# Kernel optimization log

Measured on AMD Instinct MI355X. Metric: run time of the kernel, lower is better.

The kernel has to match this reference:

```python
import jax, jax.numpy as jnp
import numpy as np

N_NODES = 2000
GCN_OUT = 8
HID = 256
N_STEPS_OUT = 4


def setup_inputs() -> dict:
    key = jax.random.key(0)
    ks = jax.random.split(key, 16)
    B, S, N, E, F, H = 32, 24, N_NODES, 16000, GCN_OUT, HID
    I = F * N  # LSTM input size = gcn_out_features * num_nodes
    s = 0.05
    inp = {
        "x_sequences": jax.random.normal(ks[0], (B, S, N), jnp.float32),
        "edge_index": jax.random.randint(ks[1], (B, S, 2, E), 0, N, jnp.int32),
        "edge_distances": jax.random.uniform(ks[2], (B, S, E), jnp.float32),
        # CustomGCNLayer params (linear 1->F)
        "W_gcn": jax.random.normal(ks[3], (1, F), jnp.float32) * s,
        "b_gcn": jnp.zeros((F,), jnp.float32),
        # 2-layer LSTM (PyTorch layout: [4H, in], gate order i,f,g,o)
        "Wih0": jax.random.normal(ks[4], (4 * H, I), jnp.float32) * s,
        "Whh0": jax.random.normal(ks[5], (4 * H, H), jnp.float32) * s,
        "bih0": jnp.zeros((4 * H,), jnp.float32),
        "bhh0": jnp.zeros((4 * H,), jnp.float32),
        "Wih1": jax.random.normal(ks[6], (4 * H, H), jnp.float32) * s,
        "Whh1": jax.random.normal(ks[7], (4 * H, H), jnp.float32) * s,
        "bih1": jnp.zeros((4 * H,), jnp.float32),
        "bhh1": jnp.zeros((4 * H,), jnp.float32),
        # fc: hidden -> n_steps_out * num_nodes * num_node_features
        "fc_W": jax.random.normal(ks[8], (N_STEPS_OUT * N, H), jnp.float32) * s,
        "fc_b": jnp.zeros((N_STEPS_OUT * N,), jnp.float32),
    }
    return inp


def _lstm_layer(x, Wih, Whh, bih, bhh):
    # x: [B, S, in] -> hs: [B, S, H]
    B = x.shape[0]
    H = Whh.shape[1]
    b = bih + bhh

    def step(carry, xt):
        h, c = carry
        gates = xt @ Wih.T + h @ Whh.T + b  # [B, 4H]
        i, f, g, o = jnp.split(gates, 4, axis=-1)
        i = jax.nn.sigmoid(i)
        f = jax.nn.sigmoid(f)
        g = jnp.tanh(g)
        o = jax.nn.sigmoid(o)
        c = f * c + i * g
        h = o * jnp.tanh(c)
        return (h, c), h

    init = (jnp.zeros((B, H), x.dtype), jnp.zeros((B, H), x.dtype))
    _, hs = jax.lax.scan(step, init, x.transpose(1, 0, 2))  # time-major
    return hs.transpose(1, 0, 2)


def reference(x_sequences, edge_index, edge_distances, W_gcn, b_gcn,
              Wih0, Whh0, bih0, bhh0, Wih1, Whh1, bih1, bhh1, fc_W, fc_b):
    B, S, N = x_sequences.shape
    F = W_gcn.shape[1]
    # GCN layer (batched over all B*S graph snapshots):
    # h = x @ W + b ; out[i] = sum_{(j->i)} dist_e * h[j]
    h = x_sequences[..., None] * W_gcn[0] + b_gcn        # [B,S,N,F]
    src = edge_index[:, :, 0].reshape(B * S, -1)         # [BS,E]
    dst = edge_index[:, :, 1].reshape(B * S, -1)
    dist = edge_distances.reshape(B * S, -1)
    h2 = h.reshape(B * S, N, F)
    msgs = jnp.take_along_axis(h2, src[:, :, None], axis=1) * dist[..., None]  # [BS,E,F]
    agg = jax.vmap(lambda m, d: jax.ops.segment_sum(m, d, num_segments=N))(msgs, dst)
    gcn_seq = jnp.tanh(agg.reshape(B, S, N * F))         # [B,S,N*F]

    h1 = _lstm_layer(gcn_seq, Wih0, Whh0, bih0, bhh0)
    h2l = _lstm_layer(h1, Wih1, Whh1, bih1, bhh1)
    last = jnp.tanh(h2l)[:, -1, :]                       # [B,H]
    out = last @ fc_W.T + fc_b                           # [B, n_steps_out*N]
    n_steps_out = fc_b.shape[0] // N
    return out.reshape(B, n_steps_out, N)                # num_node_features=1 squeezed
```

## Files before the change

kernel.cpp:

```cpp
#include <hip/hip_runtime.h>

#define DEVINL __device__ __forceinline__

typedef __attribute__((ext_vector_type(8))) short bf16x8;
typedef __attribute__((ext_vector_type(4))) float f32x4;
typedef _Float16 half2_t __attribute__((ext_vector_type(2)));
typedef _Float16 f16x8 __attribute__((ext_vector_type(8)));

DEVINL unsigned short f2bf(float f) {
  unsigned int u = __float_as_uint(f);
  u += 0x7FFFu + ((u >> 16) & 1u);
  return (unsigned short)(u >> 16);
}
DEVINL unsigned short f2h(float f) {
  return __builtin_bit_cast(unsigned short, (_Float16)f);
}
DEVINL float sigmf(float x) { return 1.f / (1.f + __expf(-x)); }
DEVINL float tanh_fast(float x) { float e = __expf(2.f * x); return 1.f - 2.f / (e + 1.f); }

DEVINL float fdot2u(unsigned int h, unsigned int w, float acc) {
  return __builtin_amdgcn_fdot2(__builtin_bit_cast(half2_t, h),
                                __builtin_bit_cast(half2_t, w), acc, false);
}

DEVINL void gload_lds16(const void* g, void* l) {
  __builtin_amdgcn_global_load_lds(
      (const __attribute__((address_space(1))) void*)g,
      (__attribute__((address_space(3))) void*)l, 16, 0, 0);
}

#define FXSCALE 1048576.f
#define FXINV   (1.f / 1048576.f)

__global__ __launch_bounds__(1024) void fused_pre(
    const float* __restrict__ x, const int* __restrict__ ei, const float* __restrict__ ed,
    const float* __restrict__ Wg, const float* __restrict__ bg,
    unsigned short* __restrict__ G,
    const float* __restrict__ Wih0, unsigned short* __restrict__ W0bf,
    const float* __restrict__ Whh0, uint2* __restrict__ WPG0,
    const float* __restrict__ Whh1, uint2* __restrict__ WPG1,
    const float* __restrict__ Wih1, unsigned short* __restrict__ W1h) {
  __shared__ float xs[2000];
  __shared__ int Ai[2000];
  __shared__ int Di[2000];
  int blk = blockIdx.x;
  int tid = threadIdx.x;

  if (blk < 768) {
    int bs = blk;
    for (int i = tid; i < 2000; i += 1024) {
      xs[i] = x[(size_t)bs * 2000 + i];
      Ai[i] = 0; Di[i] = 0;
    }
    bool bgz = (bg[0] == 0.f) && (bg[1] == 0.f) && (bg[2] == 0.f) && (bg[3] == 0.f) &&
               (bg[4] == 0.f) && (bg[5] == 0.f) && (bg[6] == 0.f) && (bg[7] == 0.f);
    __syncthreads();
    const int4* srcp = (const int4*)(ei + (size_t)bs * 32000);
    const int4* dstp = (const int4*)(ei + (size_t)bs * 32000 + 16000);
    const float4* dp = (const float4*)(ed + (size_t)bs * 16000);
    if (bgz) {
      for (int i = tid; i < 4000; i += 1024) {
        int4 s4 = srcp[i];
        int4 d4 = dstp[i];
        float4 w4 = dp[i];
        atomicAdd(&Ai[d4.x], __float2int_rn(w4.x * xs[s4.x] * FXSCALE));
        atomicAdd(&Ai[d4.y], __float2int_rn(w4.y * xs[s4.y] * FXSCALE));
        atomicAdd(&Ai[d4.z], __float2int_rn(w4.z * xs[s4.z] * FXSCALE));
        atomicAdd(&Ai[d4.w], __float2int_rn(w4.w * xs[s4.w] * FXSCALE));
      }
    } else {
      for (int i = tid; i < 4000; i += 1024) {
        int4 s4 = srcp[i];
        int4 d4 = dstp[i];
        float4 w4 = dp[i];
        atomicAdd(&Ai[d4.x], __float2int_rn(w4.x * xs[s4.x] * FXSCALE));
        atomicAdd(&Di[d4.x], __float2int_rn(w4.x * FXSCALE));
        atomicAdd(&Ai[d4.y], __float2int_rn(w4.y * xs[s4.y] * FXSCALE));
        atomicAdd(&Di[d4.y], __float2int_rn(w4.y * FXSCALE));
        atomicAdd(&Ai[d4.z], __float2int_rn(w4.z * xs[s4.z] * FXSCALE));
        atomicAdd(&Di[d4.z], __float2int_rn(w4.z * FXSCALE));
        atomicAdd(&Ai[d4.w], __float2int_rn(w4.w * xs[s4.w] * FXSCALE));
        atomicAdd(&Di[d4.w], __float2int_rn(w4.w * FXSCALE));
      }
    }
    __syncthreads();
    float wreg[8], breg[8];
#pragma unroll
    for (int f = 0; f < 8; ++f) { wreg[f] = Wg[f]; breg[f] = bg[f]; }
    for (int n = tid; n < 2000; n += 1024) {
      float a  = (float)Ai[n] * FXINV;
      float dd = (float)Di[n] * FXINV;
      unsigned int u[4];
#pragma unroll
      for (int p = 0; p < 4; ++p) {
        float v0 = tanh_fast(wreg[2 * p] * a + breg[2 * p] * dd);
        float v1 = tanh_fast(wreg[2 * p + 1] * a + breg[2 * p + 1] * dd);
        u[p] = (unsigned int)f2bf(v0) | ((unsigned int)f2bf(v1) << 16);
      }
      *(uint4*)&G[(size_t)bs * 16000 + n * 8] = make_uint4(u[0], u[1], u[2], u[3]);
    }
  } else if (blk < 1768) {
    int base = (blk - 768) * 1024 + tid;
#pragma unroll
    for (int k = 0; k < 4; ++k) {
      int id = base + k * 1024000;
      float4 v = *(const float4*)&Wih0[(size_t)id * 4];
      unsigned int a = (unsigned int)f2bf(v.x) | ((unsigned int)f2bf(v.y) << 16);
      unsigned int b = (unsigned int)f2bf(v.z) | ((unsigned int)f2bf(v.w) << 16);
      *(uint2*)&W0bf[(size_t)id * 4] = make_uint2(a, b);
    }
  } else if (blk < 1896) {
    const float* in = (blk < 1832) ? Whh0 : Whh1;
    uint2* outp = (blk < 1832) ? WPG0 : WPG1;
    int id = ((blk < 1832) ? (blk - 1768) : (blk - 1832)) * 1024 + tid;
    int g = id >> 14;
    int rem = id & 16383;
    int u2 = rem >> 8;
    int c = rem & 255;
    int col = (c >> 6) * 256 + g * 64 + (c & 63);
    float4 v = *(const float4*)&in[col * 256 + u2 * 4];
    unsigned int p0 = (unsigned int)f2h(v.x) | ((unsigned int)f2h(v.y) << 16);
    unsigned int p1 = (unsigned int)f2h(v.z) | ((unsigned int)f2h(v.w) << 16);
    outp[id] = make_uint2(p0, p1);
  } else {
    int id = (blk - 1896) * 1024 + tid;
    W1h[id] = f2h(Wih1[id]);
  }
}

__global__ __launch_bounds__(256) void gemm_bt(
    const unsigned short* __restrict__ A, const unsigned short* __restrict__ B,
    float* __restrict__ Cp) {
  __shared__ __align__(16) unsigned short As[2][128 * 32];
  __shared__ __align__(16) unsigned short Bs[2][128 * 32];
  const int K = 16000;
  int nt = blockIdx.x;
  int mt = blockIdx.y;
  int ks = blockIdx.z;
  int m0 = mt * 128, n0 = nt * 128;
  int tid = threadIdx.x;
  int lane = tid & 63;
  int w = tid >> 6;
  int wm = (w >> 1) * 64, wn = (w & 1) * 64;
  int fr = lane & 15;
  int kg = lane >> 4;

  f32x4 acc[4][4] = {};
  const unsigned short* Ag = A + (size_t)m0 * K + ks * 1600;
  const unsigned short* Bg = B + (size_t)n0 * K + ks * 1600;

  int row0 = tid >> 2,            ko0 = (tid & 3) * 8,        cb0 = (tid & ~63);
  int row1 = (256 + tid) >> 2,    ko1 = (tid & 3) * 8,        cb1 = 256 + (tid & ~63);

#define STAGE_BT(buf, kk)                                                     \
  do {                                                                        \
    gload_lds16(&Ag[(size_t)row0 * K + (kk) + ko0], &As[buf][cb0 * 8]);       \
    gload_lds16(&Bg[(size_t)row0 * K + (kk) + ko0], &Bs[buf][cb0 * 8]);       \
    gload_lds16(&Ag[(size_t)row1 * K + (kk) + ko1], &As[buf][cb1 * 8]);       \
    gload_lds16(&Bg[(size_t)row1 * K + (kk) + ko1], &Bs[buf][cb1 * 8]);       \
  } while (0)

  STAGE_BT(0, 0);
#pragma unroll 1
  for (int it = 0; it < 50; ++it) {
    int cur = it & 1;
    if (it < 49) {
      STAGE_BT(cur ^ 1, (it + 1) * 32);
      asm volatile("s_waitcnt vmcnt(4)" ::: "memory");
    } else {
      asm volatile("s_waitcnt vmcnt(0)" ::: "memory");
    }
    __builtin_amdgcn_s_barrier();
    __builtin_amdgcn_sched_barrier(0);
    bf16x8 aF[4], bF[4];
#pragma unroll
    for (int i = 0; i < 4; ++i)
      aF[i] = *(const bf16x8*)&As[cur][(wm + i * 16 + fr) * 32 + kg * 8];
#pragma unroll
    for (int i = 0; i < 4; ++i)
      bF[i] = *(const bf16x8*)&Bs[cur][(wn + i * 16 + fr) * 32 + kg * 8];
#pragma unroll
    for (int i = 0; i < 4; ++i)
#pragma unroll
      for (int j = 0; j < 4; ++j)
        acc[i][j] = __builtin_amdgcn_mfma_f32_16x16x32_bf16(aF[i], bF[j], acc[i][j], 0, 0, 0);
    __builtin_amdgcn_s_barrier();
  }
#undef STAGE_BT
  float* Co = Cp + (size_t)ks * 768 * 1024;
  int mr = (lane >> 4) * 4;
#pragma unroll
  for (int i = 0; i < 4; ++i)
#pragma unroll
    for (int j = 0; j < 4; ++j) {
      int n = n0 + wn + j * 16 + fr;
#pragma unroll
      for (int r = 0; r < 4; ++r) {
        int m = m0 + wm + i * 16 + mr + r;
        Co[(size_t)m * 1024 + n] = acc[i][j][r];
      }
    }
}

__global__ __launch_bounds__(1024) void lstm_sync2(
    const float* __restrict__ Z, const float* __restrict__ Cp,
    const float* __restrict__ bih, const float* __restrict__ bhh,
    const uint2* __restrict__ WPG,
    unsigned int* __restrict__ Hex, unsigned short* __restrict__ Hout,
    float* __restrict__ lastOut, int tagBase) {
  __shared__ __align__(16) uint2 Wl2[64 * 256];
  __shared__ float gparts[1024];
  __shared__ __align__(8) unsigned short h16[256];
  int bid = blockIdx.x;
  int b = bid & 31, g = bid >> 5;
  int tid = threadIdx.x;
  int lane = tid & 63;
  int c = tid & 255;
  int kh = __builtin_amdgcn_readfirstlane(tid >> 8);
  int q = c >> 6, r = c & 63;
  int col = q * 256 + g * 64 + r;

  const uint2* wsrc = WPG + (size_t)g * 16384;
  for (int i = tid; i < 16384; i += 1024) Wl2[i] = wsrc[i];
  if (tid < 128) ((unsigned int*)h16)[tid] = 0;
  float biasc = (Cp != nullptr && kh == 0) ? (bih[col] + bhh[col]) : 0.f;
  __syncthreads();

  float cst = 0.f;
  const size_t b24 = (size_t)b * 24;

#pragma unroll 1
  for (int t = 0; t < 24; ++t) {
    uint2 hv = *(const uint2*)&((const unsigned int*)h16)[lane * 2];
    float z = 0.f;
    if (kh == 0) {
      if (Cp != nullptr) {
        size_t off = (b24 + t) * 1024 + col;
        float s = biasc;
#pragma unroll
        for (int p = 0; p < 10; ++p) s += Cp[(size_t)p * 786432 + off];
        z = s;
      } else {
        z = Z[(b24 + t) * 1024 + col];
      }
    }
    float acc = 0.f;
#pragma unroll
    for (int j = 0; j < 16; ++j) {
      const int u2i = kh * 16 + j;
      uint2 w2 = Wl2[u2i * 256 + c];
      unsigned int h0 = (unsigned int)__builtin_amdgcn_readlane((int)hv.x, u2i);
      unsigned int h1 = (unsigned int)__builtin_amdgcn_readlane((int)hv.y, u2i);
      acc = fdot2u(h0, w2.x, acc);
      acc = fdot2u(h1, w2.y, acc);
    }
    gparts[tid] = acc + z;
    __syncthreads();
    unsigned int* HexS = Hex + (t & 1) * 8192 + b * 256;
    if (tid < 64) {
      float i_ = gparts[tid]       + gparts[tid + 256]  + gparts[tid + 512]  + gparts[tid + 768];
      float f_ = gparts[tid + 64]  + gparts[tid + 320]  + gparts[tid + 576]  + gparts[tid + 832];
      float g_ = gparts[tid + 128] + gparts[tid + 384]  + gparts[tid + 640]  + gparts[tid + 896];
      float o_ = gparts[tid + 192] + gparts[tid + 448]  + gparts[tid + 704]  + gparts[tid + 960];
      float ig = sigmf(i_), fg = sigmf(f_);
      float gg = tanh_fast(g_), og = sigmf(o_);
      cst = fg * cst + ig * gg;
      float h = og * tanh_fast(cst);
      unsigned short hh = f2h(h);
      h16[g * 64 + tid] = hh;
      __hip_atomic_store(&HexS[g * 64 + tid],
                         (unsigned int)hh | ((unsigned int)(tagBase + t + 1) << 16),
                         __ATOMIC_RELAXED, __HIP_MEMORY_SCOPE_AGENT);
      if (Hout) Hout[(b24 + t) * 256 + g * 64 + tid] = hh;
      if (lastOut && t == 23) lastOut[b * 256 + g * 64 + tid] = tanh_fast(h);
    }
    if (t == 23) break;
    if (tid < 256 && (tid >> 6) != g) {
      const unsigned int tag = (unsigned int)(tagBase + t + 1);
      unsigned int v;
      do {
        v = __hip_atomic_load(&HexS[tid], __ATOMIC_RELAXED, __HIP_MEMORY_SCOPE_AGENT);
      } while ((v >> 16) != tag);
      h16[tid] = (unsigned short)(v & 0xFFFFu);
    }
    __syncthreads();
  }
}

__global__ __launch_bounds__(256) void gemm_z1_mfma(
    const unsigned short* __restrict__ A, const unsigned short* __restrict__ B,
    const float* __restrict__ bih, const float* __restrict__ bhh,
    float* __restrict__ Z1) {
  __shared__ __align__(16) unsigned short As[128 * 32];
  __shared__ __align__(16) unsigned short Bs[128 * 32];
  const int K = 256;
  int nt = blockIdx.x;
  int mt = blockIdx.y;
  int m0 = mt * 128, n0 = nt * 128;
  int tid = threadIdx.x;
  int lane = tid & 63;
  int w = tid >> 6;
  int wm = (w >> 1) * 64, wn = (w & 1) * 64;
  int fr = lane & 15;
  int kg = lane >> 4;

  f32x4 acc[4][4] = {};
  const unsigned short* Ag = A + (size_t)m0 * K;
  const unsigned short* Bg = B + (size_t)n0 * K;

  for (int kk = 0; kk < 256; kk += 32) {
#pragma unroll
    for (int q = 0; q < 2; ++q) {
      int c = q * 256 + tid;
      int row = c >> 2;
      int ko = (c & 3) * 8;
      int cb = q * 256 + (tid & ~63);
      gload_lds16(&Ag[(size_t)row * K + kk + ko], &As[cb * 8]);
      gload_lds16(&Bg[(size_t)row * K + kk + ko], &Bs[cb * 8]);
    }
    __syncthreads();
    f16x8 aF[4], bF[4];
#pragma unroll
    for (int i = 0; i < 4; ++i)
      aF[i] = *(const f16x8*)&As[(wm + i * 16 + fr) * 32 + kg * 8];
#pragma unroll
    for (int i = 0; i < 4; ++i)
      bF[i] = *(const f16x8*)&Bs[(wn + i * 16 + fr) * 32 + kg * 8];
#pragma unroll
    for (int i = 0; i < 4; ++i)
#pragma unroll
      for (int j = 0; j < 4; ++j)
        acc[i][j] = __builtin_amdgcn_mfma_f32_16x16x32_f16(aF[i], bF[j], acc[i][j], 0, 0, 0);
    __syncthreads();
  }
  int mr = (lane >> 4) * 4;
#pragma unroll
  for (int j = 0; j < 4; ++j) {
    int n = n0 + wn + j * 16 + fr;
    float bias = bih[n] + bhh[n];
#pragma unroll
    for (int i = 0; i < 4; ++i) {
#pragma unroll
      for (int r = 0; r < 4; ++r) {
        int m = m0 + wm + i * 16 + mr + r;
        Z1[(size_t)m * 1024 + n] = acc[i][j][r] + bias;
      }
    }
  }
}

__global__ __launch_bounds__(256) void fc_kernel(
    const float* __restrict__ last, const float* __restrict__ fcW,
    const float* __restrict__ fcb, float* __restrict__ out) {
  __shared__ float ls[8][256];
  int tid = threadIdx.x;
  int o = blockIdx.x * 256 + tid;
  int b0 = blockIdx.y * 8;
  for (int i = tid; i < 2048; i += 256)
    ls[i >> 8][i & 255] = last[(b0 + (i >> 8)) * 256 + (i & 255)];
  __syncthreads();
  if (o < 8000) {
    float acc[8] = {};
    for (int k = 0; k < 256; k += 4) {
      float4 wv = *(const float4*)&fcW[(size_t)o * 256 + k];
#pragma unroll
      for (int b = 0; b < 8; ++b)
        acc[b] += wv.x * ls[b][k] + wv.y * ls[b][k + 1] + wv.z * ls[b][k + 2] + wv.w * ls[b][k + 3];
    }
    float bias = fcb[o];
#pragma unroll
    for (int b = 0; b < 8; ++b) out[(size_t)(b0 + b) * 8000 + o] = acc[b] + bias;
  }
}

extern "C" void kernel_launch(void* const* d_in, const int* in_sizes, int n_in,
                              void* d_out, int out_size, void* d_ws, size_t ws_size,
                              hipStream_t stream) {
  const float* x    = (const float*)d_in[0];
  const int*   ei   = (const int*)d_in[1];
  const float* ed   = (const float*)d_in[2];
  const float* Wg   = (const float*)d_in[3];
  const float* bg   = (const float*)d_in[4];
  const float* Wih0 = (const float*)d_in[5];
  const float* Whh0 = (const float*)d_in[6];
  const float* bih0 = (const float*)d_in[7];
  const float* bhh0 = (const float*)d_in[8];
  const float* Wih1 = (const float*)d_in[9];
  const float* Whh1 = (const float*)d_in[10];
  const float* bih1 = (const float*)d_in[11];
  const float* bhh1 = (const float*)d_in[12];
  const float* fcW  = (const float*)d_in[13];
  const float* fcb  = (const float*)d_in[14];
  float* out = (float*)d_out;

  char* ws = (char*)d_ws;
  unsigned short* Gbf  = (unsigned short*)(ws);
  unsigned short* W0bf = (unsigned short*)(ws + 24576000);
  float* Zpart = (float*)(ws + 57344000);
  uint2* WPG0  = (uint2*)(ws + 91947008);
  uint2* WPG1  = (uint2*)(ws + 92471296);
  unsigned short* W1h = (unsigned short*)(ws + 92995584);
  unsigned short* H1  = (unsigned short*)(ws + 94044160);
  float* Z1    = (float*)(ws + 94830592);
  float* lastb = (float*)(ws + 97976320);
  unsigned int* Hex0 = (unsigned int*)(ws + 98009088);
  unsigned int* Hex1 = (unsigned int*)(ws + 98074624);

  hipMemsetAsync(Hex0, 0, 131072, stream);
  fused_pre<<<2152, 1024, 0, stream>>>(x, ei, ed, Wg, bg, Gbf,
                                       Wih0, W0bf, Whh0, WPG0, Whh1, WPG1,
                                       Wih1, (unsigned short*)W1h);
  gemm_bt<<<dim3(8, 6, 10), 256, 0, stream>>>(Gbf, W0bf, Zpart);
  lstm_sync2<<<128, 1024, 0, stream>>>(nullptr, Zpart, bih0, bhh0, WPG0,
                                       Hex0, H1, nullptr, 0);
  gemm_z1_mfma<<<dim3(8, 6), 256, 0, stream>>>(H1, W1h, bih1, bhh1, Z1);
  lstm_sync2<<<128, 1024, 0, stream>>>(Z1, nullptr, nullptr, nullptr, WPG1,
                                       Hex1, nullptr, lastb, 100);
  fc_kernel<<<dim3(32, 4), 256, 0, stream>>>(lastb, fcW, fcb, out);
}
```

Baseline: 231.2 us.

## Fuse Wih0 fp32-to-bf16 conversion into the input-projection GEMM B loads

Removes the separate pass in the preprocessing kernel that converted the 1024x16000 fp32 Wih0 into a bf16 workspace copy. The GEMM now loads fp32 B tiles into registers, converts them to bf16, and writes them to LDS itself, using an extra wait and barrier per iteration. This saves the write and reread of a 32 MB bf16 buffer. In exchange, each GEMM block reads twice as many bytes for B, Wih0 is reread by all 6 M-tile blocks in fp32, and the register-staged path with an extra barrier may pipeline less well than the direct-to-LDS loads.

Result: slower. 247.2 us (+6.9%).

```diff
diff --git a/kernel.cpp b/kernel.cpp
--- a/kernel.cpp
+++ b/kernel.cpp
@@ -36,7 +36,6 @@
     const float* __restrict__ x, const int* __restrict__ ei, const float* __restrict__ ed,
     const float* __restrict__ Wg, const float* __restrict__ bg,
     unsigned short* __restrict__ G,
-    const float* __restrict__ Wih0, unsigned short* __restrict__ W0bf,
     const float* __restrict__ Whh0, uint2* __restrict__ WPG0,
     const float* __restrict__ Whh1, uint2* __restrict__ WPG1,
     const float* __restrict__ Wih1, unsigned short* __restrict__ W1h) {
@@ -99,20 +98,10 @@
       }
       *(uint4*)&G[(size_t)bs * 16000 + n * 8] = make_uint4(u[0], u[1], u[2], u[3]);
     }
-  } else if (blk < 1768) {
-    int base = (blk - 768) * 1024 + tid;
-#pragma unroll
-    for (int k = 0; k < 4; ++k) {
-      int id = base + k * 1024000;
-      float4 v = *(const float4*)&Wih0[(size_t)id * 4];
-      unsigned int a = (unsigned int)f2bf(v.x) | ((unsigned int)f2bf(v.y) << 16);
-      unsigned int b = (unsigned int)f2bf(v.z) | ((unsigned int)f2bf(v.w) << 16);
-      *(uint2*)&W0bf[(size_t)id * 4] = make_uint2(a, b);
-    }
-  } else if (blk < 1896) {
-    const float* in = (blk < 1832) ? Whh0 : Whh1;
-    uint2* outp = (blk < 1832) ? WPG0 : WPG1;
-    int id = ((blk < 1832) ? (blk - 1768) : (blk - 1832)) * 1024 + tid;
+  } else if (blk < 896) {
+    const float* in = (blk < 832) ? Whh0 : Whh1;
+    uint2* outp = (blk < 832) ? WPG0 : WPG1;
+    int id = ((blk < 832) ? (blk - 768) : (blk - 832)) * 1024 + tid;
     int g = id >> 14;
     int rem = id & 16383;
     int u2 = rem >> 8;
@@ -123,13 +112,13 @@
     unsigned int p1 = (unsigned int)f2h(v.z) | ((unsigned int)f2h(v.w) << 16);
     outp[id] = make_uint2(p0, p1);
   } else {
-    int id = (blk - 1896) * 1024 + tid;
+    int id = (blk - 896) * 1024 + tid;
     W1h[id] = f2h(Wih1[id]);
   }
 }
 
 __global__ __launch_bounds__(256) void gemm_bt(
-    const unsigned short* __restrict__ A, const unsigned short* __restrict__ B,
+    const unsigned short* __restrict__ A, const float* __restrict__ B32,
     float* __restrict__ Cp) {
   __shared__ __align__(16) unsigned short As[2][128 * 32];
   __shared__ __align__(16) unsigned short Bs[2][128 * 32];
@@ -147,31 +136,56 @@
 
   f32x4 acc[4][4] = {};
   const unsigned short* Ag = A + (size_t)m0 * K + ks * 1600;
-  const unsigned short* Bg = B + (size_t)n0 * K + ks * 1600;
+  const float* Bg = B32 + (size_t)n0 * K + ks * 1600;
 
   int row0 = tid >> 2,            ko0 = (tid & 3) * 8,        cb0 = (tid & ~63);
-  int row1 = (256 + tid) >> 2,    ko1 = (tid & 3) * 8,        cb1 = 256 + (tid & ~63);
-
-#define STAGE_BT(buf, kk)                                                     \
+  int row1 = (256 + tid) >> 2,    cb1 = 256 + (tid & ~63);
+
+#define STAGE_A(buf, kk)                                                      \
   do {                                                                        \
     gload_lds16(&Ag[(size_t)row0 * K + (kk) + ko0], &As[buf][cb0 * 8]);       \
-    gload_lds16(&Bg[(size_t)row0 * K + (kk) + ko0], &Bs[buf][cb0 * 8]);       \
-    gload_lds16(&Ag[(size_t)row1 * K + (kk) + ko1], &As[buf][cb1 * 8]);       \
-    gload_lds16(&Bg[(size_t)row1 * K + (kk) + ko1], &Bs[buf][cb1 * 8]);       \
+    gload_lds16(&Ag[(size_t)row1 * K + (kk) + ko0], &As[buf][cb1 * 8]);       \
   } while (0)
 
-  STAGE_BT(0, 0);
+  float4 ba0, ba1, bb0, bb1;
+#define LOAD_B(kk)                                                            \
+  do {                                                                        \
+    const float* p0 = &Bg[(size_t)row0 * K + (kk) + ko0];                     \
+    const float* p1 = &Bg[(size_t)row1 * K + (kk) + ko0];                     \
+    ba0 = *(const float4*)p0; ba1 = *(const float4*)(p0 + 4);                 \
+    bb0 = *(const float4*)p1; bb1 = *(const float4*)(p1 + 4);                 \
+  } while (0)
+
+#define WRITE_B(buf)                                                          \
+  do {                                                                        \
+    uint4 w0, w1;                                                             \
+    w0.x = (unsigned)f2bf(ba0.x) | ((unsigned)f2bf(ba0.y) << 16);             \
+    w0.y = (unsigned)f2bf(ba0.z) | ((unsigned)f2bf(ba0.w) << 16);             \
+    w0.z = (unsigned)f2bf(ba1.x) | ((unsigned)f2bf(ba1.y) << 16);             \
+    w0.w = (unsigned)f2bf(ba1.z) | ((unsigned)f2bf(ba1.w) << 16);             \
+    w1.x = (unsigned)f2bf(bb0.x) | ((unsigned)f2bf(bb0.y) << 16);             \
+    w1.y = (unsigned)f2bf(bb0.z) | ((unsigned)f2bf(bb0.w) << 16);             \
+    w1.z = (unsigned)f2bf(bb1.x) | ((unsigned)f2bf(bb1.y) << 16);             \
+    w1.w = (unsigned)f2bf(bb1.z) | ((unsigned)f2bf(bb1.w) << 16);             \
+    *(uint4*)&Bs[buf][tid * 8] = w0;                                          \
+    *(uint4*)&Bs[buf][(256 + tid) * 8] = w1;                                  \
+  } while (0)
+
+  STAGE_A(0, 0);
+  LOAD_B(0);
+  asm volatile("s_waitcnt vmcnt(0)" ::: "memory");
+  WRITE_B(0);
+  asm volatile("s_waitcnt lgkmcnt(0)" ::: "memory");
+  __builtin_amdgcn_s_barrier();
+  __builtin_amdgcn_sched_barrier(0);
+
 #pragma unroll 1
   for (int it = 0; it < 50; ++it) {
     int cur = it & 1;
     if (it < 49) {
-      STAGE_BT(cur ^ 1, (it + 1) * 32);
-      asm volatile("s_waitcnt vmcnt(4)" ::: "memory");
-    } else {
-      asm volatile("s_waitcnt vmcnt(0)" ::: "memory");
-    }
-    __builtin_amdgcn_s_barrier();
-    __builtin_amdgcn_sched_barrier(0);
+      STAGE_A(cur ^ 1, (it + 1) * 32);
+      LOAD_B((it + 1) * 32);
+    }
     bf16x8 aF[4], bF[4];
 #pragma unroll
     for (int i = 0; i < 4; ++i)
@@ -185,8 +199,17 @@
       for (int j = 0; j < 4; ++j)
         acc[i][j] = __builtin_amdgcn_mfma_f32_16x16x32_bf16(aF[i], bF[j], acc[i][j], 0, 0, 0);
     __builtin_amdgcn_s_barrier();
-  }
-#undef STAGE_BT
+    if (it < 49) {
+      asm volatile("s_waitcnt vmcnt(0)" ::: "memory");
+      WRITE_B(cur ^ 1);
+      asm volatile("s_waitcnt lgkmcnt(0)" ::: "memory");
+      __builtin_amdgcn_s_barrier();
+      __builtin_amdgcn_sched_barrier(0);
+    }
+  }
+#undef STAGE_A
+#undef LOAD_B
+#undef WRITE_B
   float* Co = Cp + (size_t)ks * 768 * 1024;
   int mr = (lane >> 4) * 4;
 #pragma unroll
@@ -395,7 +418,6 @@
 
   char* ws = (char*)d_ws;
   unsigned short* Gbf  = (unsigned short*)(ws);
-  unsigned short* W0bf = (unsigned short*)(ws + 24576000);
   float* Zpart = (float*)(ws + 57344000);
   uint2* WPG0  = (uint2*)(ws + 91947008);
   uint2* WPG1  = (uint2*)(ws + 92471296);
@@ -407,10 +429,10 @@
   unsigned int* Hex1 = (unsigned int*)(ws + 98074624);
 
   hipMemsetAsync(Hex0, 0, 131072, stream);
-  fused_pre<<<2152, 1024, 0, stream>>>(x, ei, ed, Wg, bg, Gbf,
-                                       Wih0, W0bf, Whh0, WPG0, Whh1, WPG1,
+  fused_pre<<<1152, 1024, 0, stream>>>(x, ei, ed, Wg, bg, Gbf,
+                                       Whh0, WPG0, Whh1, WPG1,
                                        Wih1, (unsigned short*)W1h);
-  gemm_bt<<<dim3(8, 6, 10), 256, 0, stream>>>(Gbf, W0bf, Zpart);
+  gemm_bt<<<dim3(8, 6, 10), 256, 0, stream>>>(Gbf, Wih0, Zpart);
   lstm_sync2<<<128, 1024, 0, stream>>>(nullptr, Zpart, bih0, bhh0, WPG0,
                                        Hex0, H1, nullptr, 0);
   gemm_z1_mfma<<<dim3(8, 6), 256, 0, stream>>>(H1, W1h, bih1, bhh1, Z1);
```
